# Performance work log

Hardware: AMD Instinct MI355X
Metric: run time of the kernel (lower is better)

## Reference

```python
import jax, jax.numpy as jnp
import numpy as np

H = 8  # attention_heads


def _ln(x, w, b, eps=1e-5):
    mu = x.mean(axis=-1, keepdims=True)
    var = x.var(axis=-1, keepdims=True)
    return (x - mu) / jnp.sqrt(var + eps) * w + b


def setup_inputs() -> dict:
    key = jax.random.key(0)
    ks = jax.random.split(key, 10)
    B, T, C, U, D, P = 4, 256, 2048, 4, 512, 512
    s = 0.02
    inp = {
        "model_embed": jax.random.normal(ks[0], (B, T, D), jnp.float32),
        "context_embed_key": jax.random.normal(ks[1], (C, U, D), jnp.float32),
        "context_embed_value": jax.random.normal(ks[2], (C, D), jnp.float32),
        "ln1_w": jnp.ones((D,), jnp.float32), "ln1_b": jnp.zeros((D,), jnp.float32),
        "ln2_w": jnp.ones((D,), jnp.float32), "ln2_b": jnp.zeros((D,), jnp.float32),
        "ln3_w": jnp.ones((D,), jnp.float32), "ln3_b": jnp.zeros((D,), jnp.float32),
        "ln4_w": jnp.ones((D,), jnp.float32), "ln4_b": jnp.zeros((D,), jnp.float32),
        "wq": jax.random.normal(ks[3], (D, D), jnp.float32) * s, "bq": jnp.zeros((D,), jnp.float32),
        "wk": jax.random.normal(ks[4], (D, D), jnp.float32) * s, "bk": jnp.zeros((D,), jnp.float32),
        "wv": jax.random.normal(ks[5], (D, D), jnp.float32) * s, "bv": jnp.zeros((D,), jnp.float32),
        "wo": jax.random.normal(ks[6], (D, D), jnp.float32) * s, "bo": jnp.zeros((D,), jnp.float32),
        "wp": jax.random.normal(ks[7], (D, P), jnp.float32) * s, "bp": jnp.zeros((P,), jnp.float32),
    }
    return inp


def reference(model_embed, context_embed_key, context_embed_value,
              ln1_w, ln1_b, ln2_w, ln2_b, ln3_w, ln3_b, ln4_w, ln4_b,
              wq, bq, wk, bk, wv, bv, wo, bo, wp, bp):
    B, T, D = model_embed.shape
    C, U, _ = context_embed_key.shape
    dk = D // H
    # pre-attention LayerNorms (norm_before_x1/x2/x3)
    q = _ln(model_embed, ln1_w, ln1_b)
    k = _ln(context_embed_key, ln2_w, ln2_b)
    v = _ln(context_embed_value, ln3_w, ln3_b)
    # q/k/v projections, split heads
    q = (q @ wq + bq).reshape(B, T, H, dk)
    k = (k @ wk + bk).reshape(C, U, H, dk)
    v = (v @ wv + bv).reshape(C, H, dk)
    # ColBERT late interaction: score every query token against every
    # context vector, MaxSim over the U vectors of each context entry.
    scores = jnp.einsum('bthd,cuhd->bhtcu', q, k) / jnp.sqrt(jnp.asarray(dk, q.dtype))
    scores = scores.max(axis=-1)                 # [B,H,T,C]
    attn = jax.nn.softmax(scores, axis=-1)       # softmax over contexts C
    out = jnp.einsum('bhtc,chd->bthd', attn, v).reshape(B, T, D)
    out = out @ wo + bo                          # attention output proj
    out = _ln(out, ln4_w, ln4_b)                 # norm_after
    return out @ wp + bp                         # final proj -> [B,T,P]
```

## Files before the change

### kernel.cpp

```cpp
#include <hip/hip_runtime.h>
#include <hip/hip_bf16.h>

using bf16 = __hip_bfloat16;

#define D_DIM 512
#define C_DIM 2048
#define U_DIM 4
#define DK 64

typedef __attribute__((ext_vector_type(8))) short short8;
typedef __attribute__((ext_vector_type(8))) unsigned short ushort8;
typedef __attribute__((ext_vector_type(4))) float f32x4;

__device__ __forceinline__ float dload(const void* p, size_t i, int f) {
    return f ? ((const float*)p)[i] : __bfloat162float(((const bf16*)p)[i]);
}
__device__ __forceinline__ unsigned f2bf(float x) {
    bf16 b = __float2bfloat16(x);
    return (unsigned)*(unsigned short*)&b;
}
__device__ __forceinline__ float bf2f(unsigned short us) {
    unsigned u = ((unsigned)us) << 16;
    return __builtin_bit_cast(float, u);
}

__device__ __forceinline__ int block_detect(const void* __restrict__ x) {
    __shared__ int sred[4];
    const bf16* xb = (const bf16*)x;
    int tid = threadIdx.x;
    int cnt = 0;
    #pragma unroll
    for (int i = 0; i < 4; ++i) {
        ushort8 a = *(const ushort8*)(xb + (size_t)(i * 256 + tid) * 8);
        #pragma unroll
        for (int j = 0; j < 8; ++j) {
            float v = fabsf(bf2f(a[j]));
            if (!(v <= 100.0f)) cnt++;
        }
    }
    #pragma unroll
    for (int o = 32; o > 0; o >>= 1) cnt += __shfl_down(cnt, o);
    if ((tid & 63) == 0) sred[tid >> 6] = cnt;
    __syncthreads();
    int c = sred[0] + sred[1] + sred[2] + sred[3];
    return (c > 400) ? 1 : 0;
}

template <bool LN, bool XF, bool WF>
__device__ __forceinline__ void pack_a_body(const void* __restrict__ X,
                                            const void* __restrict__ lnw,
                                            const void* __restrict__ lnb,
                                            uint4* __restrict__ Af, int tt) {
    int m = threadIdx.x >> 4;
    int kbL = threadIdx.x & 15;
    int row = tt * 16 + m;
    float v[32];
    float s = 0.0f, ss = 0.0f;
    #pragma unroll
    for (int i = 0; i < 4; ++i) {
        int k0 = (kbL + i * 16) * 8;
        if constexpr (XF) {
            const float4* p = (const float4*)((const float*)X + (size_t)row * D_DIM + k0);
            float4 a = p[0], b = p[1];
            v[i*8+0] = a.x; v[i*8+1] = a.y; v[i*8+2] = a.z; v[i*8+3] = a.w;
            v[i*8+4] = b.x; v[i*8+5] = b.y; v[i*8+6] = b.z; v[i*8+7] = b.w;
        } else {
            ushort8 a = *(const ushort8*)((const bf16*)X + (size_t)row * D_DIM + k0);
            #pragma unroll
            for (int j = 0; j < 8; ++j) v[i*8+j] = bf2f(a[j]);
        }
        #pragma unroll
        for (int j = 0; j < 8; ++j) { float x = v[i*8+j]; s += x; ss += x * x; }
    }
    float mu = 0.0f, rs = 1.0f;
    if (LN) {
        #pragma unroll
        for (int o = 1; o < 16; o <<= 1) { s += __shfl_xor(s, o); ss += __shfl_xor(ss, o); }
        mu = s * (1.0f / D_DIM);
        float var = ss * (1.0f / D_DIM) - mu * mu;
        rs = rsqrtf(var + 1e-5f);
    }
    #pragma unroll
    for (int i = 0; i < 4; ++i) {
        int kb = kbL + i * 16;
        int k0 = kb * 8;
        float lw[8], lb[8];
        if (LN) {
            if constexpr (WF) {
                const float4* pw = (const float4*)((const float*)lnw + k0);
                const float4* pb = (const float4*)((const float*)lnb + k0);
                float4 w0 = pw[0], w1 = pw[1], b0 = pb[0], b1 = pb[1];
                lw[0]=w0.x; lw[1]=w0.y; lw[2]=w0.z; lw[3]=w0.w;
                lw[4]=w1.x; lw[5]=w1.y; lw[6]=w1.z; lw[7]=w1.w;
                lb[0]=b0.x; lb[1]=b0.y; lb[2]=b0.z; lb[3]=b0.w;
                lb[4]=b1.x; lb[5]=b1.y; lb[6]=b1.z; lb[7]=b1.w;
            } else {
                ushort8 w8 = *(const ushort8*)((const bf16*)lnw + k0);
                ushort8 b8 = *(const ushort8*)((const bf16*)lnb + k0);
                #pragma unroll
                for (int j = 0; j < 8; ++j) { lw[j] = bf2f(w8[j]); lb[j] = bf2f(b8[j]); }
            }
        }
        unsigned pk[4];
        #pragma unroll
        for (int jp = 0; jp < 4; ++jp) {
            float v0 = v[i * 8 + jp * 2];
            float v1 = v[i * 8 + jp * 2 + 1];
            if (LN) {
                v0 = (v0 - mu) * rs * lw[jp * 2] + lb[jp * 2];
                v1 = (v1 - mu) * rs * lw[jp * 2 + 1] + lb[jp * 2 + 1];
            }
            pk[jp] = f2bf(v0) | (f2bf(v1) << 16);
        }
        uint4 wv = {pk[0], pk[1], pk[2], pk[3]};
        Af[((size_t)tt * 64 + kb) * 16 + m] = wv;
    }
}

template <bool LN>
__global__ __launch_bounds__(256, 1)
void pack_a_kernel(const void* __restrict__ X, int x_raw,
                   const void* __restrict__ lnw, const void* __restrict__ lnb,
                   uint4* __restrict__ Af, const int* __restrict__ flagp) {
    int f = *flagp;
    (void)x_raw;
    if (f) pack_a_body<LN, true, true>(X, lnw, lnb, Af, blockIdx.x);
    else   pack_a_body<LN, true, false>(X, lnw, lnb, Af, blockIdx.x);
}

template <bool WF>
__device__ __forceinline__ void pack_w_body(const void* __restrict__ W,
                                            uint4* __restrict__ Bf, int b,
                                            float (*t)[65]) {
    int n0 = (b & 7) * 64, k0 = (b >> 3) * 64;
    int tid = threadIdx.x;
    if constexpr (WF) {
        #pragma unroll
        for (int i = 0; i < 4; ++i) {
            int e = i * 256 + tid;
            int r = e >> 4, c = (e & 15) * 4;
            float4 a = *(const float4*)((const float*)W + (size_t)(k0 + r) * D_DIM + n0 + c);
            t[r][c] = a.x; t[r][c+1] = a.y; t[r][c+2] = a.z; t[r][c+3] = a.w;
        }
    } else {
        #pragma unroll
        for (int i = 0; i < 2; ++i) {
            int e = i * 256 + tid;
            int r = e >> 3, c = (e & 7) * 8;
            ushort8 a = *(const ushort8*)((const bf16*)W + (size_t)(k0 + r) * D_DIM + n0 + c);
            #pragma unroll
            for (int j = 0; j < 8; ++j) t[r][c + j] = bf2f(a[j]);
        }
    }
    __syncthreads();
    #pragma unroll
    for (int i = 0; i < 2; ++i) {
        int e = i * 256 + tid;
        int nl = e & 63, kbl = e >> 6;
        unsigned pk[4];
        #pragma unroll
        for (int jp = 0; jp < 4; ++jp)
            pk[jp] = f2bf(t[kbl * 8 + jp * 2][nl]) | (f2bf(t[kbl * 8 + jp * 2 + 1][nl]) << 16);
        uint4 wv = {pk[0], pk[1], pk[2], pk[3]};
        int n = n0 + nl;
        Bf[(((size_t)(n >> 4)) * 64 + (k0 / 8 + kbl)) * 16 + (n & 15)] = wv;
    }
}

__global__ __launch_bounds__(256, 1)
void pack_all_kernel(const void* __restrict__ me, const void* __restrict__ l1w, const void* __restrict__ l1b,
                     const void* __restrict__ ck, const void* __restrict__ l2w, const void* __restrict__ l2b,
                     const void* __restrict__ cv, const void* __restrict__ l3w, const void* __restrict__ l3b,
                     uint4* __restrict__ Aq, uint4* __restrict__ Ak, uint4* __restrict__ Av,
                     const void* W0, const void* W1, const void* W2,
                     const void* W3, const void* W4,
                     uint4* B0, uint4* B1, uint4* B2, uint4* B3, uint4* B4,
                     int* __restrict__ flagp) {
    __shared__ float t[64][65];
    int f = block_detect(me);
    if (blockIdx.x == 0 && threadIdx.x == 0) *flagp = f;
    int b = blockIdx.x;
    const void* Ws[5] = {W0, W1, W2, W3, W4};
    uint4* Bs[5] = {B0, B1, B2, B3, B4};
    if (f) {
        if (b < 64)       pack_a_body<true, true, true>(me, l1w, l1b, Aq, b);
        else if (b < 576) pack_a_body<true, true, true>(ck, l2w, l2b, Ak, b - 64);
        else if (b < 704) pack_a_body<true, true, true>(cv, l3w, l3b, Av, b - 576);
        else { int c = b - 704; pack_w_body<true>(Ws[c >> 6], Bs[c >> 6], c & 63, t); }
    } else {
        if (b < 64)       pack_a_body<true, false, false>(me, l1w, l1b, Aq, b);
        else if (b < 576) pack_a_body<true, false, false>(ck, l2w, l2b, Ak, b - 64);
        else if (b < 704) pack_a_body<true, false, false>(cv, l3w, l3b, Av, b - 576);
        else { int c = b - 704; pack_w_body<false>(Ws[c >> 6], Bs[c >> 6], c & 63, t); }
    }
}

template <int OUT>
__device__ __forceinline__ void mfma_gemm_body(const uint4* __restrict__ Af,
                                               const uint4* __restrict__ Bf,
                                               const void* __restrict__ bias,
                                               float* __restrict__ Y,
                                               uint4* __restrict__ Fout, int Rtt,
                                               int f, int bx, int by,
                                               float (*t)[65]) {
    int w = threadIdx.x >> 6, lane = threadIdx.x & 63;
    int q = lane >> 4, mn = lane & 15;
    int mt = by * 4 + w;
    int nt0 = bx * 4;
    f32x4 acc[4] = {{0.f,0.f,0.f,0.f},{0.f,0.f,0.f,0.f},{0.f,0.f,0.f,0.f},{0.f,0.f,0.f,0.f}};
    for (int kw = 0; kw < 16; ++kw) {
        short8 a = *(const short8*)(Af + ((size_t)mt * 64 + kw * 4 + q) * 16 + mn);
        #pragma unroll
        for (int i = 0; i < 4; ++i) {
            short8 b = *(const short8*)(Bf + (((size_t)(nt0 + i)) * 64 + kw * 4 + q) * 16 + mn);
            acc[i] = __builtin_amdgcn_mfma_f32_16x16x32_bf16(a, b, acc[i], 0, 0, 0);
        }
    }
    if constexpr (OUT == 0) {
        #pragma unroll
        for (int i = 0; i < 4; ++i) {
            int col = (nt0 + i) * 16 + mn;
            float bv = dload(bias, col, f);
            #pragma unroll
            for (int r = 0; r < 4; ++r)
                Y[(size_t)(mt * 16 + q * 4 + r) * D_DIM + col] = acc[i][r] + bv;
        }
    } else {
        #pragma unroll
        for (int i = 0; i < 4; ++i) {
            float bv = dload(bias, (nt0 + i) * 16 + mn, f);
            #pragma unroll
            for (int r = 0; r < 4; ++r)
                t[w * 16 + q * 4 + r][i * 16 + mn] = acc[i][r] + bv;
        }
        __syncthreads();
        int h = bx;
        if constexpr (OUT == 1) {
            #pragma unroll
            for (int e0 = 0; e0 < 2; ++e0) {
                int e = e0 * 256 + threadIdx.x;
                int m = e & 15, kb = (e >> 4) & 7, ttl = e >> 7;
                const float* src = &t[ttl * 16 + m][kb * 8];
                uint4 wv;
                wv.x = f2bf(src[0]) | (f2bf(src[1]) << 16);
                wv.y = f2bf(src[2]) | (f2bf(src[3]) << 16);
                wv.z = f2bf(src[4]) | (f2bf(src[5]) << 16);
                wv.w = f2bf(src[6]) | (f2bf(src[7]) << 16);
                Fout[(((size_t)h * Rtt + by * 4 + ttl) * 8 + kb) * 16 + m] = wv;
            }
        } else if constexpr (OUT == 2) {
            #pragma unroll
            for (int e0 = 0; e0 < 2; ++e0) {
                int e = e0 * 256 + threadIdx.x;
                int lane2 = e & 63, nt = (e >> 6) & 3, ctl = e >> 8;
                int nm2 = lane2 & 15, q2 = lane2 >> 4;
                int col = nt * 16 + nm2;
                int rb = ctl * 32 + q2 * 8;
                uint4 wv;
                wv.x = f2bf(t[rb + 0][col]) | (f2bf(t[rb + 1][col]) << 16);
                wv.y = f2bf(t[rb + 2][col]) | (f2bf(t[rb + 3][col]) << 16);
                wv.z = f2bf(t[rb + 4][col]) | (f2bf(t[rb + 5][col]) << 16);
                wv.w = f2bf(t[rb + 6][col]) | (f2bf(t[rb + 7][col]) << 16);
                Fout[(((size_t)h * 64 + by * 2 + ctl) * 4 + nt) * 64 + lane2] = wv;
            }
        } else {
            #pragma unroll
            for (int e0 = 0; e0 < 2; ++e0) {
                int e = e0 * 256 + threadIdx.x;
                int m2 = e & 15, kb = (e >> 4) & 7, u = e >> 7;
                const float* src = &t[m2 * 4 + u][kb * 8];
                uint4 wv;
                wv.x = f2bf(src[0]) | (f2bf(src[1]) << 16);
                wv.y = f2bf(src[2]) | (f2bf(src[3]) << 16);
                wv.z = f2bf(src[4]) | (f2bf(src[5]) << 16);
                wv.w = f2bf(src[6]) | (f2bf(src[7]) << 16);
                int nt = by * 4 + u;
                Fout[(((size_t)h * 512 + nt) * 8 + kb) * 16 + m2] = wv;
            }
        }
    }
}

template <int OUT>
__global__ __launch_bounds__(256, 1)
void mfma_gemm_kernel(const uint4* __restrict__ Af, const uint4* __restrict__ Bf,
                      const void* __restrict__ bias, float* __restrict__ Y,
                      uint4* __restrict__ Fout, int Rtt,
                      const int* __restrict__ flagp) {
    __shared__ float t[64][65];
    mfma_gemm_body<OUT>(Af, Bf, bias, Y, Fout, Rtt, *flagp, blockIdx.x, blockIdx.y, t);
}

__global__ __launch_bounds__(256, 1)
void gemm_qkv_kernel(const uint4* __restrict__ Aq, const uint4* __restrict__ Ak,
                     const uint4* __restrict__ Av,
                     const uint4* __restrict__ wfq, const uint4* __restrict__ wfk,
                     const uint4* __restrict__ wfv,
                     const void* __restrict__ bq, const void* __restrict__ bk,
                     const void* __restrict__ bv,
                     uint4* __restrict__ qf, uint4* __restrict__ kf,
                     uint4* __restrict__ vf,
                     const int* __restrict__ flagp) {
    __shared__ float t[64][65];
    int f = *flagp;
    int b = blockIdx.x;
    if (b < 1024) {
        mfma_gemm_body<3>(Ak, wfk, bk, nullptr, kf, 512, f, b & 7, b >> 3, t);
    } else if (b < 1280) {
        int c = b - 1024;
        mfma_gemm_body<2>(Av, wfv, bv, nullptr, vf, 0, f, c & 7, c >> 3, t);
    } else {
        int c = b - 1280;
        mfma_gemm_body<1>(Aq, wfq, bq, nullptr, qf, 64, f, c & 7, c >> 3, t);
    }
}

__global__ __launch_bounds__(256, 1)
void attn_fused_kernel(const uint4* __restrict__ qf, const uint4* __restrict__ kf,
                       const uint4* __restrict__ vf,
                       float* __restrict__ pacc, float* __restrict__ pm,
                       float* __restrict__ pl) {
    __shared__ float sp[4][16][36];
    int tid = threadIdx.x;
    int w = tid >> 6, lane = tid & 63;
    int q = lane >> 4, nm = lane & 15;
    int b = blockIdx.x;
    int s = b & 7;
    int h = (b >> 3) & 7;
    int qb = b >> 6;
    int mt = qb * 4 + w;

    short8 a0 = *(const short8*)(qf + (((size_t)h * 64 + mt) * 8 + q) * 16 + nm);
    short8 a1 = *(const short8*)(qf + (((size_t)h * 64 + mt) * 8 + 4 + q) * 16 + nm);

    f32x4 sc[8][2];
    #pragma unroll
    for (int st = 0; st < 8; ++st) {
        #pragma unroll
        for (int hh = 0; hh < 2; ++hh) {
            int ct16 = (s * 8 + st) * 2 + hh;
            f32x4 scv = {-1e30f, -1e30f, -1e30f, -1e30f};
            __builtin_amdgcn_s_setprio(1);
            #pragma unroll
            for (int u = 0; u < 4; ++u) {
                int nt = ct16 * 4 + u;
                short8 b0 = *(const short8*)(kf + (((size_t)h * 512 + nt) * 8 + q) * 16 + nm);
                short8 b1 = *(const short8*)(kf + (((size_t)h * 512 + nt) * 8 + 4 + q) * 16 + nm);
                f32x4 acc = {0.0f, 0.0f, 0.0f, 0.0f};
                acc = __builtin_amdgcn_mfma_f32_16x16x32_bf16(a0, b0, acc, 0, 0, 0);
                acc = __builtin_amdgcn_mfma_f32_16x16x32_bf16(a1, b1, acc, 0, 0, 0);
                #pragma unroll
                for (int r = 0; r < 4; ++r) scv[r] = fmaxf(scv[r], acc[r]);
            }
            __builtin_amdgcn_s_setprio(0);
            #pragma unroll
            for (int r = 0; r < 4; ++r) sc[st][hh][r] = scv[r] * 0.125f;
        }
    }

    float mrow[4], lrow[4];
    #pragma unroll
    for (int r = 0; r < 4; ++r) {
        float m = sc[0][0][r];
        #pragma unroll
        for (int st = 0; st < 8; ++st) {
            m = fmaxf(m, sc[st][0][r]);
            m = fmaxf(m, sc[st][1][r]);
        }
        m = fmaxf(m, __shfl_xor(m, 1));
        m = fmaxf(m, __shfl_xor(m, 2));
        m = fmaxf(m, __shfl_xor(m, 4));
        m = fmaxf(m, __shfl_xor(m, 8));
        mrow[r] = m;
        lrow[r] = 0.0f;
    }

    f32x4 acc_o[4] = {{0.f,0.f,0.f,0.f},{0.f,0.f,0.f,0.f},{0.f,0.f,0.f,0.f},{0.f,0.f,0.f,0.f}};
    #pragma unroll
    for (int st = 0; st < 8; ++st) {
        #pragma unroll
        for (int r = 0; r < 4; ++r) {
            float p0 = __expf(sc[st][0][r] - mrow[r]);
            float p1 = __expf(sc[st][1][r] - mrow[r]);
            sp[w][q * 4 + r][nm] = p0;
            sp[w][q * 4 + r][16 + nm] = p1;
            lrow[r] += p0 + p1;
        }
        float4 pa0 = *(const float4*)&sp[w][nm][q * 8];
        float4 pa1 = *(const float4*)&sp[w][nm][q * 8 + 4];
        uint4 av;
        av.x = f2bf(pa0.x) | (f2bf(pa0.y) << 16);
        av.y = f2bf(pa0.z) | (f2bf(pa0.w) << 16);
        av.z = f2bf(pa1.x) | (f2bf(pa1.y) << 16);
        av.w = f2bf(pa1.z) | (f2bf(pa1.w) << 16);
        short8 ap = *(short8*)&av;
        int ct32 = s * 8 + st;
        __builtin_amdgcn_s_setprio(1);
        #pragma unroll
        for (int nt2 = 0; nt2 < 4; ++nt2) {
            short8 bv = *(const short8*)(vf + (((size_t)h * 64 + ct32) * 4 + nt2) * 64 + lane);
            acc_o[nt2] = __builtin_amdgcn_mfma_f32_16x16x32_bf16(ap, bv, acc_o[nt2], 0, 0, 0);
        }
        __builtin_amdgcn_s_setprio(0);
    }

    #pragma unroll
    for (int r = 0; r < 4; ++r) {
        float ps = lrow[r];
        ps += __shfl_xor(ps, 1);
        ps += __shfl_xor(ps, 2);
        ps += __shfl_xor(ps, 4);
        ps += __shfl_xor(ps, 8);
        lrow[r] = ps;
    }

    int p_idx = ((qb * 8 + h) << 3) + s;
    float* po = pacc + ((size_t)p_idx * 64 + w * 16) * 64;
    #pragma unroll
    for (int nt2 = 0; nt2 < 4; ++nt2)
        #pragma unroll
        for (int r = 0; r < 4; ++r)
            po[(q * 4 + r) * 64 + nt2 * 16 + nm] = acc_o[nt2][r];
    if (nm == 0) {
        #pragma unroll
        for (int r = 0; r < 4; ++r) {
            pm[p_idx * 64 + w * 16 + q * 4 + r] = mrow[r];
            pl[p_idx * 64 + w * 16 + q * 4 + r] = lrow[r];
        }
    }
}

__global__ void attn_merge2_kernel(const float* __restrict__ pacc, const float* __restrict__ pm,
                                   const float* __restrict__ pl, uint4* __restrict__ oAf) {
    int b = blockIdx.x;
    int qb = b >> 3, h = b & 7;
    int tid = threadIdx.x;
    int t_loc = tid & 63, dg = tid >> 6;
    int p0 = b * 8;
    float M = -1e30f;
    #pragma unroll
    for (int s = 0; s < 8; ++s) M = fmaxf(M, pm[(p0 + s) * 64 + t_loc]);
    float L = 0.0f;
    float4 o[4] = {};
    #pragma unroll
    for (int s = 0; s < 8; ++s) {
        float e = __expf(pm[(p0 + s) * 64 + t_loc] - M);
        L += pl[(p0 + s) * 64 + t_loc] * e;
        const float4* po = (const float4*)(pacc + ((size_t)(p0 + s) * 64 + t_loc) * 64 + dg * 16);
        #pragma unroll
        for (int d = 0; d < 4; ++d) {
            float4 v = po[d];
            o[d].x += v.x * e; o[d].y += v.y * e; o[d].z += v.z * e; o[d].w += v.w * e;
        }
    }
    float inv = 1.0f / L;
    int t = qb * 64 + t_loc;
    int tt = t >> 4, m = t & 15;
    int kb0 = h * 8 + dg * 2;
    uint4 u0, u1;
    u0.x = f2bf(o[0].x * inv) | (f2bf(o[0].y * inv) << 16);
    u0.y = f2bf(o[0].z * inv) | (f2bf(o[0].w * inv) << 16);
    u0.z = f2bf(o[1].x * inv) | (f2bf(o[1].y * inv) << 16);
    u0.w = f2bf(o[1].z * inv) | (f2bf(o[1].w * inv) << 16);
    u1.x = f2bf(o[2].x * inv) | (f2bf(o[2].y * inv) << 16);
    u1.y = f2bf(o[2].z * inv) | (f2bf(o[2].w * inv) << 16);
    u1.z = f2bf(o[3].x * inv) | (f2bf(o[3].y * inv) << 16);
    u1.w = f2bf(o[3].z * inv) | (f2bf(o[3].w * inv) << 16);
    oAf[((size_t)tt * 64 + kb0) * 16 + m] = u0;
    oAf[((size_t)tt * 64 + kb0 + 1) * 16 + m] = u1;
}

extern "C" void kernel_launch(void* const* d_in, const int* in_sizes, int n_in,
                              void* d_out, int out_size, void* d_ws, size_t ws_size,
                              hipStream_t stream) {
    const void* model_embed = d_in[0];
    const void* ctx_key     = d_in[1];
    const void* ctx_val     = d_in[2];
    const void* ln1w = d_in[3];  const void* ln1b = d_in[4];
    const void* ln2w = d_in[5];  const void* ln2b = d_in[6];
    const void* ln3w = d_in[7];  const void* ln3b = d_in[8];
    const void* ln4w = d_in[9];  const void* ln4b = d_in[10];
    const void* wq = d_in[11];   const void* bq = d_in[12];
    const void* wk = d_in[13];   const void* bk = d_in[14];
    const void* wv = d_in[15];   const void* bv = d_in[16];
    const void* wo = d_in[17];   const void* bo = d_in[18];
    const void* wp = d_in[19];   const void* bp = d_in[20];

    int*   flagp = (int*)d_ws;
    float* ws    = (float*)d_ws + 16;
    float* o1    = ws;
    float* qTf   = o1 + 524288;
    float* kTf   = qTf + 262144;
    float* Aqf   = kTf + 2097152;
    float* Akf   = Aqf + 262144;
    float* Avf   = Akf + 2097152;
    float* vff   = Avf + 524288;
    float* pacc2 = vff + 524288;
    float* pm2   = pacc2 + 4194304;
    float* pl2   = pm2 + 65536;
    float* wfr   = pl2 + 65536;

    uint4* qf  = (uint4*)qTf;
    uint4* kf  = (uint4*)kTf;
    uint4* Aq  = (uint4*)Aqf;
    uint4* Ak  = (uint4*)Akf;
    uint4* Av  = (uint4*)Avf;
    uint4* vf  = (uint4*)vff;
    uint4* oAf = (uint4*)vff;
    uint4* wfq = (uint4*)wfr;
    uint4* wfk = wfq + 32768;
    uint4* wfv = wfk + 32768;
    uint4* wfo = wfv + 32768;
    uint4* wfp = wfo + 32768;

    pack_all_kernel<<<1024, 256, 0, stream>>>(model_embed, ln1w, ln1b,
                                              ctx_key, ln2w, ln2b,
                                              ctx_val, ln3w, ln3b,
                                              Aq, Ak, Av,
                                              wq, wk, wv, wo, wp,
                                              wfq, wfk, wfv, wfo, wfp, flagp);

    gemm_qkv_kernel<<<1408, 256, 0, stream>>>(Aq, Ak, Av, wfq, wfk, wfv,
                                              bq, bk, bv, qf, kf, vf, flagp);

    attn_fused_kernel<<<1024, 256, 0, stream>>>(qf, kf, vf, pacc2, pm2, pl2);
    attn_merge2_kernel<<<128, 256, 0, stream>>>(pacc2, pm2, pl2, oAf);

    mfma_gemm_kernel<0><<<dim3(8, 16), 256, 0, stream>>>(oAf, wfo, bo, o1, nullptr, 0, flagp);
    pack_a_kernel<true><<<64, 256, 0, stream>>>(o1, 0, ln4w, ln4b, Aq, flagp);
    mfma_gemm_kernel<0><<<dim3(8, 16), 256, 0, stream>>>(Aq, wfp, bp, (float*)d_out, nullptr, 0, flagp);

    (void)ws_size;
}
```

Baseline: 195.6 us.

## Fuse attention merge, output projection, LayerNorm and final projection into one kernel

```diff
diff --git a/kernel.cpp b/kernel.cpp
--- a/kernel.cpp
+++ b/kernel.cpp
@@ -115,17 +115,6 @@
         uint4 wv = {pk[0], pk[1], pk[2], pk[3]};
         Af[((size_t)tt * 64 + kb) * 16 + m] = wv;
     }
-}
-
-template <bool LN>
-__global__ __launch_bounds__(256, 1)
-void pack_a_kernel(const void* __restrict__ X, int x_raw,
-                   const void* __restrict__ lnw, const void* __restrict__ lnb,
-                   uint4* __restrict__ Af, const int* __restrict__ flagp) {
-    int f = *flagp;
-    (void)x_raw;
-    if (f) pack_a_body<LN, true, true>(X, lnw, lnb, Af, blockIdx.x);
-    else   pack_a_body<LN, true, false>(X, lnw, lnb, Af, blockIdx.x);
 }
 
 template <bool WF>
@@ -199,7 +188,6 @@
 __device__ __forceinline__ void mfma_gemm_body(const uint4* __restrict__ Af,
                                                const uint4* __restrict__ Bf,
                                                const void* __restrict__ bias,
-                                               float* __restrict__ Y,
                                                uint4* __restrict__ Fout, int Rtt,
                                                int f, int bx, int by,
                                                float (*t)[65]) {
@@ -216,79 +204,58 @@
             acc[i] = __builtin_amdgcn_mfma_f32_16x16x32_bf16(a, b, acc[i], 0, 0, 0);
         }
     }
-    if constexpr (OUT == 0) {
-        #pragma unroll
-        for (int i = 0; i < 4; ++i) {
-            int col = (nt0 + i) * 16 + mn;
-            float bv = dload(bias, col, f);
-            #pragma unroll
-            for (int r = 0; r < 4; ++r)
-                Y[(size_t)(mt * 16 + q * 4 + r) * D_DIM + col] = acc[i][r] + bv;
+    #pragma unroll
+    for (int i = 0; i < 4; ++i) {
+        float bv = dload(bias, (nt0 + i) * 16 + mn, f);
+        #pragma unroll
+        for (int r = 0; r < 4; ++r)
+            t[w * 16 + q * 4 + r][i * 16 + mn] = acc[i][r] + bv;
+    }
+    __syncthreads();
+    int h = bx;
+    if constexpr (OUT == 1) {
+        #pragma unroll
+        for (int e0 = 0; e0 < 2; ++e0) {
+            int e = e0 * 256 + threadIdx.x;
+            int m = e & 15, kb = (e >> 4) & 7, ttl = e >> 7;
+            const float* src = &t[ttl * 16 + m][kb * 8];
+            uint4 wv;
+            wv.x = f2bf(src[0]) | (f2bf(src[1]) << 16);
+            wv.y = f2bf(src[2]) | (f2bf(src[3]) << 16);
+            wv.z = f2bf(src[4]) | (f2bf(src[5]) << 16);
+            wv.w = f2bf(src[6]) | (f2bf(src[7]) << 16);
+            Fout[(((size_t)h * Rtt + by * 4 + ttl) * 8 + kb) * 16 + m] = wv;
+        }
+    } else if constexpr (OUT == 2) {
+        #pragma unroll
+        for (int e0 = 0; e0 < 2; ++e0) {
+            int e = e0 * 256 + threadIdx.x;
+            int lane2 = e & 63, nt = (e >> 6) & 3, ctl = e >> 8;
+            int nm2 = lane2 & 15, q2 = lane2 >> 4;
+            int col = nt * 16 + nm2;
+            int rb = ctl * 32 + q2 * 8;
+            uint4 wv;
+            wv.x = f2bf(t[rb + 0][col]) | (f2bf(t[rb + 1][col]) << 16);
+            wv.y = f2bf(t[rb + 2][col]) | (f2bf(t[rb + 3][col]) << 16);
+            wv.z = f2bf(t[rb + 4][col]) | (f2bf(t[rb + 5][col]) << 16);
+            wv.w = f2bf(t[rb + 6][col]) | (f2bf(t[rb + 7][col]) << 16);
+            Fout[(((size_t)h * 64 + by * 2 + ctl) * 4 + nt) * 64 + lane2] = wv;
         }
     } else {
         #pragma unroll
-        for (int i = 0; i < 4; ++i) {
-            float bv = dload(bias, (nt0 + i) * 16 + mn, f);
-            #pragma unroll
-            for (int r = 0; r < 4; ++r)
-                t[w * 16 + q * 4 + r][i * 16 + mn] = acc[i][r] + bv;
-        }
-        __syncthreads();
-        int h = bx;
-        if constexpr (OUT == 1) {
-            #pragma unroll
-            for (int e0 = 0; e0 < 2; ++e0) {
-                int e = e0 * 256 + threadIdx.x;
-                int m = e & 15, kb = (e >> 4) & 7, ttl = e >> 7;
-                const float* src = &t[ttl * 16 + m][kb * 8];
-                uint4 wv;
-                wv.x = f2bf(src[0]) | (f2bf(src[1]) << 16);
-                wv.y = f2bf(src[2]) | (f2bf(src[3]) << 16);
-                wv.z = f2bf(src[4]) | (f2bf(src[5]) << 16);
-                wv.w = f2bf(src[6]) | (f2bf(src[7]) << 16);
-                Fout[(((size_t)h * Rtt + by * 4 + ttl) * 8 + kb) * 16 + m] = wv;
-            }
-        } else if constexpr (OUT == 2) {
-            #pragma unroll
-            for (int e0 = 0; e0 < 2; ++e0) {
-                int e = e0 * 256 + threadIdx.x;
-                int lane2 = e & 63, nt = (e >> 6) & 3, ctl = e >> 8;
-                int nm2 = lane2 & 15, q2 = lane2 >> 4;
-                int col = nt * 16 + nm2;
-                int rb = ctl * 32 + q2 * 8;
-                uint4 wv;
-                wv.x = f2bf(t[rb + 0][col]) | (f2bf(t[rb + 1][col]) << 16);
-                wv.y = f2bf(t[rb + 2][col]) | (f2bf(t[rb + 3][col]) << 16);
-                wv.z = f2bf(t[rb + 4][col]) | (f2bf(t[rb + 5][col]) << 16);
-                wv.w = f2bf(t[rb + 6][col]) | (f2bf(t[rb + 7][col]) << 16);
-                Fout[(((size_t)h * 64 + by * 2 + ctl) * 4 + nt) * 64 + lane2] = wv;
-            }
-        } else {
-            #pragma unroll
-            for (int e0 = 0; e0 < 2; ++e0) {
-                int e = e0 * 256 + threadIdx.x;
-                int m2 = e & 15, kb = (e >> 4) & 7, u = e >> 7;
-                const float* src = &t[m2 * 4 + u][kb * 8];
-                uint4 wv;
-                wv.x = f2bf(src[0]) | (f2bf(src[1]) << 16);
-                wv.y = f2bf(src[2]) | (f2bf(src[3]) << 16);
-                wv.z = f2bf(src[4]) | (f2bf(src[5]) << 16);
-                wv.w = f2bf(src[6]) | (f2bf(src[7]) << 16);
-                int nt = by * 4 + u;
-                Fout[(((size_t)h * 512 + nt) * 8 + kb) * 16 + m2] = wv;
-            }
-        }
-    }
-}
-
-template <int OUT>
-__global__ __launch_bounds__(256, 1)
-void mfma_gemm_kernel(const uint4* __restrict__ Af, const uint4* __restrict__ Bf,
-                      const void* __restrict__ bias, float* __restrict__ Y,
-                      uint4* __restrict__ Fout, int Rtt,
-                      const int* __restrict__ flagp) {
-    __shared__ float t[64][65];
-    mfma_gemm_body<OUT>(Af, Bf, bias, Y, Fout, Rtt, *flagp, blockIdx.x, blockIdx.y, t);
+        for (int e0 = 0; e0 < 2; ++e0) {
+            int e = e0 * 256 + threadIdx.x;
+            int m2 = e & 15, kb = (e >> 4) & 7, u = e >> 7;
+            const float* src = &t[m2 * 4 + u][kb * 8];
+            uint4 wv;
+            wv.x = f2bf(src[0]) | (f2bf(src[1]) << 16);
+            wv.y = f2bf(src[2]) | (f2bf(src[3]) << 16);
+            wv.z = f2bf(src[4]) | (f2bf(src[5]) << 16);
+            wv.w = f2bf(src[6]) | (f2bf(src[7]) << 16);
+            int nt = by * 4 + u;
+            Fout[(((size_t)h * 512 + nt) * 8 + kb) * 16 + m2] = wv;
+        }
+    }
 }
 
 __global__ __launch_bounds__(256, 1)
@@ -305,13 +272,13 @@
     int f = *flagp;
     int b = blockIdx.x;
     if (b < 1024) {
-        mfma_gemm_body<3>(Ak, wfk, bk, nullptr, kf, 512, f, b & 7, b >> 3, t);
+        mfma_gemm_body<3>(Ak, wfk, bk, kf, 512, f, b & 7, b >> 3, t);
     } else if (b < 1280) {
         int c = b - 1024;
-        mfma_gemm_body<2>(Av, wfv, bv, nullptr, vf, 0, f, c & 7, c >> 3, t);
+        mfma_gemm_body<2>(Av, wfv, bv, vf, 0, f, c & 7, c >> 3, t);
     } else {
         int c = b - 1280;
-        mfma_gemm_body<1>(Aq, wfq, bq, nullptr, qf, 64, f, c & 7, c >> 3, t);
+        mfma_gemm_body<1>(Aq, wfq, bq, qf, 64, f, c & 7, c >> 3, t);
     }
 }
 
@@ -430,44 +397,158 @@
     }
 }
 
-__global__ void attn_merge2_kernel(const float* __restrict__ pacc, const float* __restrict__ pm,
-                                   const float* __restrict__ pl, uint4* __restrict__ oAf) {
-    int b = blockIdx.x;
-    int qb = b >> 3, h = b & 7;
+__global__ __launch_bounds__(256, 1)
+void tail_kernel(const float* __restrict__ pacc, const float* __restrict__ pm,
+                 const float* __restrict__ pl,
+                 const uint4* __restrict__ wfo, const uint4* __restrict__ wfp,
+                 const void* __restrict__ bo, const void* __restrict__ bp,
+                 const void* __restrict__ ln4w, const void* __restrict__ ln4b,
+                 float* __restrict__ Y, const int* __restrict__ flagp) {
+    __shared__ uint4 lfr[64][16];
+    __shared__ float xs[4][16][132];
+    __shared__ float lw4[512], lb4[512];
+    __shared__ float sred[4][16][2];
+    int f = *flagp;
     int tid = threadIdx.x;
-    int t_loc = tid & 63, dg = tid >> 6;
-    int p0 = b * 8;
-    float M = -1e30f;
-    #pragma unroll
-    for (int s = 0; s < 8; ++s) M = fmaxf(M, pm[(p0 + s) * 64 + t_loc]);
-    float L = 0.0f;
-    float4 o[4] = {};
-    #pragma unroll
-    for (int s = 0; s < 8; ++s) {
-        float e = __expf(pm[(p0 + s) * 64 + t_loc] - M);
-        L += pl[(p0 + s) * 64 + t_loc] * e;
-        const float4* po = (const float4*)(pacc + ((size_t)(p0 + s) * 64 + t_loc) * 64 + dg * 16);
-        #pragma unroll
-        for (int d = 0; d < 4; ++d) {
-            float4 v = po[d];
-            o[d].x += v.x * e; o[d].y += v.y * e; o[d].z += v.z * e; o[d].w += v.w * e;
-        }
-    }
-    float inv = 1.0f / L;
-    int t = qb * 64 + t_loc;
-    int tt = t >> 4, m = t & 15;
-    int kb0 = h * 8 + dg * 2;
-    uint4 u0, u1;
-    u0.x = f2bf(o[0].x * inv) | (f2bf(o[0].y * inv) << 16);
-    u0.y = f2bf(o[0].z * inv) | (f2bf(o[0].w * inv) << 16);
-    u0.z = f2bf(o[1].x * inv) | (f2bf(o[1].y * inv) << 16);
-    u0.w = f2bf(o[1].z * inv) | (f2bf(o[1].w * inv) << 16);
-    u1.x = f2bf(o[2].x * inv) | (f2bf(o[2].y * inv) << 16);
-    u1.y = f2bf(o[2].z * inv) | (f2bf(o[2].w * inv) << 16);
-    u1.z = f2bf(o[3].x * inv) | (f2bf(o[3].y * inv) << 16);
-    u1.w = f2bf(o[3].z * inv) | (f2bf(o[3].w * inv) << 16);
-    oAf[((size_t)tt * 64 + kb0) * 16 + m] = u0;
-    oAf[((size_t)tt * 64 + kb0 + 1) * 16 + m] = u1;
+    int rt = blockIdx.x;
+    int qb = rt >> 2;
+    int row64base = (rt & 3) * 16;
+
+    for (int i = tid; i < 512; i += 256) { lw4[i] = dload(ln4w, i, f); lb4[i] = dload(ln4b, i, f); }
+
+    {
+        int row16 = tid >> 4;
+        int seg   = tid & 15;
+        int h = seg >> 1, half = seg & 1;
+        int t_loc = row64base + row16;
+        int p0 = (qb * 8 + h) << 3;
+        float M = -1e30f;
+        #pragma unroll
+        for (int s = 0; s < 8; ++s) M = fmaxf(M, pm[(p0 + s) * 64 + t_loc]);
+        float L = 0.0f;
+        float4 o[8] = {};
+        #pragma unroll
+        for (int s = 0; s < 8; ++s) {
+            float e = __expf(pm[(p0 + s) * 64 + t_loc] - M);
+            L += pl[(p0 + s) * 64 + t_loc] * e;
+            const float4* po = (const float4*)(pacc + ((size_t)(p0 + s) * 64 + t_loc) * 64 + half * 32);
+            #pragma unroll
+            for (int d = 0; d < 8; ++d) {
+                float4 v = po[d];
+                o[d].x += v.x * e; o[d].y += v.y * e; o[d].z += v.z * e; o[d].w += v.w * e;
+            }
+        }
+        float inv = 1.0f / L;
+        #pragma unroll
+        for (int j = 0; j < 4; ++j) {
+            uint4 u;
+            u.x = f2bf(o[j*2].x * inv)   | (f2bf(o[j*2].y * inv) << 16);
+            u.y = f2bf(o[j*2].z * inv)   | (f2bf(o[j*2].w * inv) << 16);
+            u.z = f2bf(o[j*2+1].x * inv) | (f2bf(o[j*2+1].y * inv) << 16);
+            u.w = f2bf(o[j*2+1].z * inv) | (f2bf(o[j*2+1].w * inv) << 16);
+            lfr[h * 8 + half * 4 + j][row16] = u;
+        }
+    }
+    __syncthreads();
+
+    int w = tid >> 6, lane = tid & 63;
+    int q = lane >> 4, mn = lane & 15;
+    f32x4 acc[8];
+    #pragma unroll
+    for (int i = 0; i < 8; ++i) acc[i] = {0.f, 0.f, 0.f, 0.f};
+    for (int kw = 0; kw < 16; ++kw) {
+        short8 a = *(const short8*)&lfr[kw * 4 + q][mn];
+        #pragma unroll
+        for (int i = 0; i < 8; ++i) {
+            int nt = w * 8 + i;
+            short8 b = *(const short8*)(wfo + ((size_t)nt * 64 + kw * 4 + q) * 16 + mn);
+            acc[i] = __builtin_amdgcn_mfma_f32_16x16x32_bf16(a, b, acc[i], 0, 0, 0);
+        }
+    }
+    #pragma unroll
+    for (int i = 0; i < 8; ++i) {
+        float bv = dload(bo, (w * 8 + i) * 16 + mn, f);
+        #pragma unroll
+        for (int r = 0; r < 4; ++r) acc[i][r] += bv;
+    }
+
+    {
+        float ps[4], pq[4];
+        #pragma unroll
+        for (int r = 0; r < 4; ++r) {
+            float s = 0.f, sq = 0.f;
+            #pragma unroll
+            for (int i = 0; i < 8; ++i) { float x = acc[i][r]; s += x; sq += x * x; }
+            #pragma unroll
+            for (int o = 1; o < 16; o <<= 1) { s += __shfl_xor(s, o); sq += __shfl_xor(sq, o); }
+            ps[r] = s; pq[r] = sq;
+        }
+        if (mn == 0) {
+            #pragma unroll
+            for (int r = 0; r < 4; ++r) { sred[w][q*4+r][0] = ps[r]; sred[w][q*4+r][1] = pq[r]; }
+        }
+    }
+    __syncthreads();
+
+    float mu[4], rs[4];
+    #pragma unroll
+    for (int r = 0; r < 4; ++r) {
+        int rr = q * 4 + r;
+        float s  = sred[0][rr][0] + sred[1][rr][0] + sred[2][rr][0] + sred[3][rr][0];
+        float sq = sred[0][rr][1] + sred[1][rr][1] + sred[2][rr][1] + sred[3][rr][1];
+        mu[r] = s * (1.0f / D_DIM);
+        float var = sq * (1.0f / D_DIM) - mu[r] * mu[r];
+        rs[r] = rsqrtf(var + 1e-5f);
+    }
+
+    #pragma unroll
+    for (int i = 0; i < 8; ++i) {
+        int col = w * 128 + i * 16 + mn;
+        float g = lw4[col], bb = lb4[col];
+        #pragma unroll
+        for (int r = 0; r < 4; ++r) {
+            float x = (acc[i][r] - mu[r]) * rs[r] * g + bb;
+            xs[w][q * 4 + r][i * 16 + mn] = x;
+        }
+    }
+    __syncthreads();
+
+    #pragma unroll
+    for (int it = 0; it < 4; ++it) {
+        int m = mn;
+        int kbl = q + it * 4;
+        const float* src = &xs[w][m][kbl * 8];
+        float4 s0 = *(const float4*)src;
+        float4 s1 = *(const float4*)(src + 4);
+        uint4 u;
+        u.x = f2bf(s0.x) | (f2bf(s0.y) << 16);
+        u.y = f2bf(s0.z) | (f2bf(s0.w) << 16);
+        u.z = f2bf(s1.x) | (f2bf(s1.y) << 16);
+        u.w = f2bf(s1.z) | (f2bf(s1.w) << 16);
+        lfr[w * 16 + kbl][m] = u;
+    }
+    __syncthreads();
+
+    f32x4 acc2[8];
+    #pragma unroll
+    for (int i = 0; i < 8; ++i) acc2[i] = {0.f, 0.f, 0.f, 0.f};
+    for (int kw = 0; kw < 16; ++kw) {
+        short8 a = *(const short8*)&lfr[kw * 4 + q][mn];
+        #pragma unroll
+        for (int i = 0; i < 8; ++i) {
+            int nt = w * 8 + i;
+            short8 b = *(const short8*)(wfp + ((size_t)nt * 64 + kw * 4 + q) * 16 + mn);
+            acc2[i] = __builtin_amdgcn_mfma_f32_16x16x32_bf16(a, b, acc2[i], 0, 0, 0);
+        }
+    }
+    #pragma unroll
+    for (int i = 0; i < 8; ++i) {
+        int col = w * 128 + i * 16 + mn;
+        float bv = dload(bp, col, f);
+        #pragma unroll
+        for (int r = 0; r < 4; ++r)
+            Y[(size_t)(rt * 16 + q * 4 + r) * D_DIM + col] = acc2[i][r] + bv;
+    }
 }
 
 extern "C" void kernel_launch(void* const* d_in, const int* in_sizes, int n_in,
@@ -506,7 +587,6 @@
     uint4* Ak  = (uint4*)Akf;
     uint4* Av  = (uint4*)Avf;
     uint4* vf  = (uint4*)vff;
-    uint4* oAf = (uint4*)vff;
     uint4* wfq = (uint4*)wfr;
     uint4* wfk = wfq + 32768;
     uint4* wfv = wfk + 32768;
@@ -524,11 +604,10 @@
                                               bq, bk, bv, qf, kf, vf, flagp);
 
     attn_fused_kernel<<<1024, 256, 0, stream>>>(qf, kf, vf, pacc2, pm2, pl2);
-    attn_merge2_kernel<<<128, 256, 0, stream>>>(pacc2, pm2, pl2, oAf);
-
-    mfma_gemm_kernel<0><<<dim3(8, 16), 256, 0, stream>>>(oAf, wfo, bo, o1, nullptr, 0, flagp);
-    pack_a_kernel<true><<<64, 256, 0, stream>>>(o1, 0, ln4w, ln4b, Aq, flagp);
-    mfma_gemm_kernel<0><<<dim3(8, 16), 256, 0, stream>>>(Aq, wfp, bp, (float*)d_out, nullptr, 0, flagp);
+
+    tail_kernel<<<64, 256, 0, stream>>>(pacc2, pm2, pl2, wfo, wfp,
+                                        bo, bp, ln4w, ln4b,
+                                        (float*)d_out, flagp);
 
     (void)ws_size;
 }
```

Result: slower. 207.7 us (+6.2%).
